# Kernel optimization log

Measured on AMD Instinct MI355X. Metric: run time of the kernel, lower is better.

## Reference

```python
import jax, jax.numpy as jnp
import numpy as np
import math

IN_F, OUT_F = 4096, 4096
ORDER, TENSOR_RANK = 4, 8
LEAF_A = math.ceil(IN_F ** (1.0 / ORDER))   # 8
LEAF_B = math.ceil(OUT_F ** (1.0 / ORDER))  # 8


def setup_inputs() -> dict:
    key = jax.random.key(0)
    k1, k2, k3, k4 = jax.random.split(key, 4)
    x = jax.random.normal(k1, (8, 2048, IN_F), dtype=jnp.float32)
    weight = jax.random.normal(k2, (OUT_F, IN_F), dtype=jnp.float32) * 0.02
    bias = jax.random.normal(k3, (OUT_F,), dtype=jnp.float32) * 0.02
    # reset_parameters: gain for leaky_relu(sqrt(5)) = sqrt(2/(1+5)); std = gain / in_features**(1/order)
    gain = math.sqrt(2.0 / (1.0 + 5.0))
    std = gain / (IN_F ** (1.0 / ORDER))
    weight_leafs = jax.random.uniform(
        k4, (ORDER, TENSOR_RANK, LEAF_A, LEAF_B), dtype=jnp.float32,
        minval=-std, maxval=std)
    return {"x": x, "weight": weight, "bias": bias, "weight_leafs": weight_leafs}


def _reproduce_weight(weight_leafs):
    # Original einsum 'lij,rmn->rimjn' sums the FIRST operand over its leading
    # (rank) axis; chained through both stages + final .sum(0), every leaf is
    # summed over tensor_rank. Exact math = nested Kronecker of the rank-summed
    # leaves, sliced to [:in_features, :out_features].
    s = weight_leafs.sum(axis=1)  # (4, a, b)
    a, b = LEAF_A, LEAF_B
    z1 = jnp.einsum('ij,mn->imjn', s[0], s[1]).reshape(a * a, b * b)
    z2 = jnp.einsum('ij,mn->imjn', s[2], s[3]).reshape(a * a, b * b)
    zzz = jnp.einsum('ij,mn->imjn', z1, z2).reshape(a ** 4, b ** 4)
    return zzz[:IN_F, :OUT_F]  # (in_features, out_features)


def reference(x, weight, bias, weight_leafs):
    tensor_weight = _reproduce_weight(weight_leafs)       # (in, out)
    full_weight = weight + tensor_weight.T                # (out, in)
    # F.linear: x @ W^T + b
    return jnp.einsum('bsi,oi->bso', x, full_weight) + bias
```

## Files before the change

### kernel.cpp

```cpp
#include <hip/hip_runtime.h>
#include <hip/hip_bf16.h>
#include <stdint.h>

typedef __attribute__((ext_vector_type(8))) __bf16 bf16x8;
typedef __attribute__((ext_vector_type(4))) float f32x4;

#define IN_F   4096
#define OUT_F  4096
#define M_ROWS 16384

static __device__ __forceinline__ unsigned short f2bf(float f) {
    unsigned int u = __float_as_uint(f);
    u += 0x7FFFu + ((u >> 16) & 1u);
    return (unsigned short)(u >> 16);
}

__global__ __launch_bounds__(256) void build_w_kernel(
    const float* __restrict__ weight, const float* __restrict__ leafs,
    unsigned short* __restrict__ wb)
{
    __shared__ float s[4][8][8];
    const int t = threadIdx.x;
    {
        const int o = t >> 6, a = (t >> 3) & 7, b = t & 7;
        float acc = 0.f;
        #pragma unroll
        for (int r = 0; r < 8; ++r)
            acc += leafs[o * 512 + r * 64 + a * 8 + b];
        s[o][a][b] = acc;
    }
    __syncthreads();

    const int total = (OUT_F * IN_F) / 8;
    for (int idx = blockIdx.x * 256 + t; idx < total; idx += gridDim.x * 256) {
        const int n  = idx >> 9;
        const int kg = idx & 511;
        const int n0 = n >> 9, n1 = (n >> 6) & 7, n2 = (n >> 3) & 7, n3 = n & 7;
        const int k0 = kg >> 6, k1 = (kg >> 3) & 7, k2 = kg & 7;
        const float p = s[0][k0][n0] * s[1][k1][n1] * s[2][k2][n2];
        const float4* wp = (const float4*)(weight + (size_t)n * IN_F + kg * 8);
        const float4 w0 = wp[0], w1 = wp[1];
        const float wv[8] = {w0.x, w0.y, w0.z, w0.w, w1.x, w1.y, w1.z, w1.w};
        unsigned int pk[4];
        #pragma unroll
        for (int j = 0; j < 4; ++j) {
            unsigned int lo = f2bf(wv[2*j]   + p * s[3][2*j]  [n3]);
            unsigned int hi = f2bf(wv[2*j+1] + p * s[3][2*j+1][n3]);
            pk[j] = lo | (hi << 16);
        }
        *reinterpret_cast<uint4*>(wb + (size_t)n * IN_F + kg * 8) =
            make_uint4(pk[0], pk[1], pk[2], pk[3]);
    }
}

__global__ __launch_bounds__(256) void conv_x_kernel(
    const float* __restrict__ x, unsigned short* __restrict__ xb, long long n8)
{
    for (long long idx = (long long)blockIdx.x * 256 + threadIdx.x; idx < n8;
         idx += (long long)gridDim.x * 256) {
        const float4* xp = (const float4*)(x + idx * 8);
        const float4 a = xp[0], b = xp[1];
        const float v[8] = {a.x, a.y, a.z, a.w, b.x, b.y, b.z, b.w};
        unsigned int pk[4];
        #pragma unroll
        for (int j = 0; j < 4; ++j)
            pk[j] = (unsigned int)f2bf(v[2*j]) | ((unsigned int)f2bf(v[2*j+1]) << 16);
        *reinterpret_cast<uint4*>(xb + idx * 8) = make_uint4(pk[0], pk[1], pk[2], pk[3]);
    }
}

#define BK 64
#define NT 64

#define PANEL_A(b,kk) (ldsb + ((b)*2+(kk))*16384)
#define PANEL_B(b,kk) (ldsb + 65536 + ((b)*2+(kk))*16384)

#define GLL(src, dst) __builtin_amdgcn_global_load_lds( \
    (const __attribute__((address_space(1))) void*)(src), \
    (__attribute__((address_space(3))) void*)(dst), 16, 0, 0)

#define STAGE_A(b, kk, ko) do { \
    GLL(sA1 + (ko) + (kk)*32,          PANEL_A(b,kk) + d1); \
    GLL(sA1 + 524288 + (ko) + (kk)*32, PANEL_A(b,kk) + d1 + 8192); } while(0)
#define STAGE_B(b, kk, ko) do { \
    GLL(sB1 + (ko) + (kk)*32,          PANEL_B(b,kk) + d1); \
    GLL(sB1 + 524288 + (ko) + (kk)*32, PANEL_B(b,kk) + d1 + 8192); } while(0)

#define SB0  __builtin_amdgcn_sched_barrier(0)
#define BAR  __builtin_amdgcn_s_barrier()
#define PRI1 __builtin_amdgcn_s_setprio(1)
#define PRI0 __builtin_amdgcn_s_setprio(0)
#define WLG4 asm volatile("s_waitcnt lgkmcnt(4)" ::: "memory")
#define WLG0 asm volatile("s_waitcnt lgkmcnt(0)" ::: "memory")
#define WVM2 asm volatile("s_waitcnt vmcnt(2)" ::: "memory")
#define WVM0 asm volatile("s_waitcnt vmcnt(0)" ::: "memory")

#define LDA(dst, BUF, KK, MH) do { _Pragma("unroll") \
    for (int i_ = 0; i_ < 4; ++i_) \
        dst[i_] = *(const bf16x8*)(aB + ((BUF)*32768 + (KK)*16384 + ((MH)*4+i_)*1024)); } while(0)
#define LDB(dst, BUF, KK) do { _Pragma("unroll") \
    for (int i_ = 0; i_ < 4; ++i_) \
        dst[i_] = *(const bf16x8*)(bB + ((BUF)*32768 + (KK)*16384 + i_*1024)); } while(0)
#define MM(AS, MH) do { _Pragma("unroll") \
    for (int m_ = 0; m_ < 4; ++m_) { _Pragma("unroll") \
    for (int n_ = 0; n_ < 4; ++n_) \
        acc[(MH)*4+m_][n_] = __builtin_amdgcn_mfma_f32_16x16x32_bf16( \
            AS[m_], bF[n_], acc[(MH)*4+m_][n_], 0, 0, 0); } } while(0)

#define TILE(BUF, KO, PF) do { \
     \
    LDB(bF, BUF, 0); \
    LDA(aQ, BUF, 0, 1); \
    if (PF) STAGE_A((BUF)^1, 0, KO); \
    SB0; WLG4; SB0; \
    PRI1; MM(aP, 0); PRI0; SB0; \
    if (PF) { WVM2; } else { WVM0; } \
    BAR; SB0; \
     \
    LDA(aP, BUF, 1, 0); \
    if (PF) STAGE_B((BUF)^1, 0, KO); \
    SB0; WLG4; SB0; \
    PRI1; MM(aQ, 1); PRI0; SB0; \
    BAR; SB0; \
     \
    LDB(bF, BUF, 1); \
    LDA(aQ, BUF, 1, 1); \
    if (PF) STAGE_A((BUF)^1, 1, KO); \
    SB0; WLG4; SB0; \
    PRI1; MM(aP, 0); PRI0; SB0; \
    if (PF) { WVM2; } else { WVM0; } \
    BAR; SB0; \
     \
    if (PF) { LDA(aP, (BUF)^1, 0, 0); STAGE_B((BUF)^1, 1, KO); SB0; WLG4; } \
    else    { SB0; WLG0; } \
    SB0; \
    PRI1; MM(aQ, 1); PRI0; SB0; \
    BAR; SB0; \
} while (0)

__global__ __launch_bounds__(512, 2) void gemm8_kernel(
    const unsigned short* __restrict__ xb,
    const unsigned short* __restrict__ wb,
    const float* __restrict__ bias,
    float* __restrict__ out)
{
    __shared__ unsigned short lds_us[65536];
    char* const ldsb = (char*)lds_us;

    const int t    = threadIdx.x;
    const int wave = t >> 6;
    const int lane = t & 63;
    const int lr   = lane & 15;
    const int kq   = lane >> 4;
    const int wr   = wave >> 2;
    const int wcn  = wave & 3;
    const int sx   = (lr & 6) << 3;

    const int bid  = blockIdx.x;
    const int swzb = (bid & 7) * 128 + (bid >> 3);
    const int bm   = (swzb >> 4) * 256;
    const int bn   = (swzb & 15) * 256;

    const int c1 = t;
    const int r1 = c1 >> 2;
    const int q1 = ((c1 & 3) * 16) ^ ((r1 & 6) << 3);
    const unsigned short* sA1 = xb + (size_t)(bm + r1) * IN_F + (q1 >> 1);
    const unsigned short* sB1 = wb + (size_t)(bn + r1) * IN_F + (q1 >> 1);
    const int d1 = c1 * 16;

    const char* aB = ldsb + (wr * 128 + lr) * 64 + ((kq * 16) ^ sx);
    const char* bB = ldsb + 65536 + (wcn * 64 + lr) * 64 + ((kq * 16) ^ sx);

    f32x4 acc[8][4] = {};
    bf16x8 aP[4], aQ[4], bF[4];

    STAGE_A(0, 0, 0); STAGE_B(0, 0, 0); STAGE_A(0, 1, 0); STAGE_B(0, 1, 0);
    asm volatile("s_waitcnt vmcnt(4)" ::: "memory");
    BAR; SB0;
    LDA(aP, 0, 0, 0);

    #pragma unroll 1
    for (int tt = 0; tt < NT - 2; tt += 2) {
        const int ko0 = (tt + 1) * BK;
        const int ko1 = (tt + 2) * BK;
        TILE(0, ko0, true);
        TILE(1, ko1, true);
    }
    TILE(0, (NT - 1) * BK, true);
    TILE(1, 0, false);

    #pragma unroll
    for (int n = 0; n < 4; ++n) {
        const int col = bn + wcn * 64 + n * 16 + lr;
        const float bv = bias[col];
        #pragma unroll
        for (int m = 0; m < 8; ++m) {
            const size_t rb = (size_t)(bm + wr * 128 + m * 16 + kq * 4) * OUT_F + col;
            #pragma unroll
            for (int j = 0; j < 4; ++j)
                out[rb + (size_t)j * OUT_F] = acc[m][n][j] + bv;
        }
    }
}

#define FBM 128
#define FBN 128
#define FBK 32

__global__ __launch_bounds__(256) void gemm_fb_kernel(
    const float* __restrict__ xf,
    const unsigned short* __restrict__ wb,
    const float* __restrict__ bias,
    float* __restrict__ out)
{
    __shared__ unsigned short As[FBM * FBK];
    __shared__ unsigned short Bs[FBN * FBK];

    const int t    = threadIdx.x;
    const int wave = t >> 6;
    const int lane = t & 63;
    const int lr   = lane & 15;
    const int kq   = lane >> 4;
    const int wr   = wave >> 1;
    const int wc   = wave & 1;

    const int bm = blockIdx.x * FBM;
    const int bn = blockIdx.y * FBN;
    const int srow = t >> 2;
    const int scol = (t & 3) * 8;

    f32x4 acc[4][4] = {};

    for (int kt = 0; kt < IN_F; kt += FBK) {
        #pragma unroll
        for (int g = 0; g < 2; ++g) {
            const int row = srow + g * 64;
            const float4* xp = (const float4*)(xf + (size_t)(bm + row) * IN_F + kt + scol);
            const float4 a0 = xp[0], a1 = xp[1];
            const float v[8] = {a0.x, a0.y, a0.z, a0.w, a1.x, a1.y, a1.z, a1.w};
            unsigned int pk[4];
            #pragma unroll
            for (int j = 0; j < 4; ++j)
                pk[j] = (unsigned int)f2bf(v[2*j]) | ((unsigned int)f2bf(v[2*j+1]) << 16);
            *reinterpret_cast<uint4*>(&As[row * FBK + scol]) =
                make_uint4(pk[0], pk[1], pk[2], pk[3]);
        }
        {
            const unsigned short* gb0 = wb + (size_t)(bn + srow) * IN_F + kt + scol;
            const unsigned short* gb1 = gb0 + (size_t)64 * IN_F;
            GLL(gb0, Bs + srow * FBK + scol);
            GLL(gb1, Bs + (64 + srow) * FBK + scol);
        }
        __syncthreads();

        bf16x8 af[4], bfr[4];
        #pragma unroll
        for (int m = 0; m < 4; ++m)
            af[m] = *reinterpret_cast<const bf16x8*>(As + (wr * 64 + m * 16 + lr) * FBK + kq * 8);
        #pragma unroll
        for (int n = 0; n < 4; ++n)
            bfr[n] = *reinterpret_cast<const bf16x8*>(Bs + (wc * 64 + n * 16 + lr) * FBK + kq * 8);

        #pragma unroll
        for (int m = 0; m < 4; ++m)
            #pragma unroll
            for (int n = 0; n < 4; ++n)
                acc[m][n] = __builtin_amdgcn_mfma_f32_16x16x32_bf16(af[m], bfr[n], acc[m][n], 0, 0, 0);

        __syncthreads();
    }

    const int crow0 = kq * 4;
    #pragma unroll
    for (int n = 0; n < 4; ++n) {
        const int col = bn + wc * 64 + n * 16 + lr;
        const float bv = bias[col];
        #pragma unroll
        for (int m = 0; m < 4; ++m) {
            const int rowb = bm + wr * 64 + m * 16 + crow0;
            #pragma unroll
            for (int j = 0; j < 4; ++j)
                out[(size_t)(rowb + j) * OUT_F + col] = acc[m][n][j] + bv;
        }
    }
}

extern "C" void kernel_launch(void* const* d_in, const int* in_sizes, int n_in,
                              void* d_out, int out_size, void* d_ws, size_t ws_size,
                              hipStream_t stream) {
    const float* x      = (const float*)d_in[0];
    const float* weight = (const float*)d_in[1];
    const float* bias   = (const float*)d_in[2];
    const float* leafs  = (const float*)d_in[3];
    float* out = (float*)d_out;

    unsigned short* wb = (unsigned short*)d_ws;
    unsigned short* xbuf = (unsigned short*)((char*)d_ws +
                           (size_t)OUT_F * IN_F * sizeof(unsigned short));

    const size_t need_full = (size_t)OUT_F * IN_F * 2 + (size_t)M_ROWS * IN_F * 2;
    const bool full = ws_size >= need_full;

    build_w_kernel<<<dim3(2048), dim3(256), 0, stream>>>(weight, leafs, wb);

    if (full) {
        conv_x_kernel<<<dim3(2048), dim3(256), 0, stream>>>(
            x, xbuf, (long long)M_ROWS * IN_F / 8);
        gemm8_kernel<<<dim3((M_ROWS / 256) * (OUT_F / 256)), dim3(512), 0, stream>>>(
            xbuf, wb, bias, out);
    } else {
        gemm_fb_kernel<<<dim3(M_ROWS / FBM, OUT_F / FBN), dim3(256), 0, stream>>>(
            x, wb, bias, out);
    }
}
```

Measured before the change: 590.2 us.

## Merge weight/x prep kernels and double-buffer B fragments in GEMM

Combines the weight-building and x-conversion kernels into one launch, with blocks split in proportion to the work so both bandwidth-bound conversions run concurrently and one launch and its tail are removed. In the GEMM main loop, B fragments now use two register sets (bP/bQ). Each B load is issued one phase earlier alongside the A loads, and the LDS wait threshold rises to lgkmcnt(8) so more loads stay in flight while MFMAs run. This adds 16 VGPRs per thread, which could pressure the 2-blocks-per-CU occupancy target.

Result: no change. 594.1 us (+0.7%).

```diff
diff --git a/kernel.cpp b/kernel.cpp
--- a/kernel.cpp
+++ b/kernel.cpp
@@ -15,57 +15,62 @@
     return (unsigned short)(u >> 16);
 }
 
-__global__ __launch_bounds__(256) void build_w_kernel(
+#define PREP_WBLK 1366
+#define PREP_NBLK 4096
+
+__global__ __launch_bounds__(256) void prep_kernel(
     const float* __restrict__ weight, const float* __restrict__ leafs,
-    unsigned short* __restrict__ wb)
+    const float* __restrict__ x,
+    unsigned short* __restrict__ wb, unsigned short* __restrict__ xbuf)
 {
-    __shared__ float s[4][8][8];
     const int t = threadIdx.x;
-    {
-        const int o = t >> 6, a = (t >> 3) & 7, b = t & 7;
-        float acc = 0.f;
-        #pragma unroll
-        for (int r = 0; r < 8; ++r)
-            acc += leafs[o * 512 + r * 64 + a * 8 + b];
-        s[o][a][b] = acc;
-    }
-    __syncthreads();
-
-    const int total = (OUT_F * IN_F) / 8;
-    for (int idx = blockIdx.x * 256 + t; idx < total; idx += gridDim.x * 256) {
-        const int n  = idx >> 9;
-        const int kg = idx & 511;
-        const int n0 = n >> 9, n1 = (n >> 6) & 7, n2 = (n >> 3) & 7, n3 = n & 7;
-        const int k0 = kg >> 6, k1 = (kg >> 3) & 7, k2 = kg & 7;
-        const float p = s[0][k0][n0] * s[1][k1][n1] * s[2][k2][n2];
-        const float4* wp = (const float4*)(weight + (size_t)n * IN_F + kg * 8);
-        const float4 w0 = wp[0], w1 = wp[1];
-        const float wv[8] = {w0.x, w0.y, w0.z, w0.w, w1.x, w1.y, w1.z, w1.w};
-        unsigned int pk[4];
-        #pragma unroll
-        for (int j = 0; j < 4; ++j) {
-            unsigned int lo = f2bf(wv[2*j]   + p * s[3][2*j]  [n3]);
-            unsigned int hi = f2bf(wv[2*j+1] + p * s[3][2*j+1][n3]);
-            pk[j] = lo | (hi << 16);
-        }
-        *reinterpret_cast<uint4*>(wb + (size_t)n * IN_F + kg * 8) =
-            make_uint4(pk[0], pk[1], pk[2], pk[3]);
-    }
-}
-
-__global__ __launch_bounds__(256) void conv_x_kernel(
-    const float* __restrict__ x, unsigned short* __restrict__ xb, long long n8)
-{
-    for (long long idx = (long long)blockIdx.x * 256 + threadIdx.x; idx < n8;
-         idx += (long long)gridDim.x * 256) {
-        const float4* xp = (const float4*)(x + idx * 8);
-        const float4 a = xp[0], b = xp[1];
-        const float v[8] = {a.x, a.y, a.z, a.w, b.x, b.y, b.z, b.w};
-        unsigned int pk[4];
-        #pragma unroll
-        for (int j = 0; j < 4; ++j)
-            pk[j] = (unsigned int)f2bf(v[2*j]) | ((unsigned int)f2bf(v[2*j+1]) << 16);
-        *reinterpret_cast<uint4*>(xb + idx * 8) = make_uint4(pk[0], pk[1], pk[2], pk[3]);
+    if (blockIdx.x < PREP_WBLK) {
+        __shared__ float s[4][8][8];
+        {
+            const int o = t >> 6, a = (t >> 3) & 7, b = t & 7;
+            float acc = 0.f;
+            #pragma unroll
+            for (int r = 0; r < 8; ++r)
+                acc += leafs[o * 512 + r * 64 + a * 8 + b];
+            s[o][a][b] = acc;
+        }
+        __syncthreads();
+
+        const int total = (OUT_F * IN_F) / 8;
+        for (int idx = blockIdx.x * 256 + t; idx < total; idx += PREP_WBLK * 256) {
+            const int n  = idx >> 9;
+            const int kg = idx & 511;
+            const int n0 = n >> 9, n1 = (n >> 6) & 7, n2 = (n >> 3) & 7, n3 = n & 7;
+            const int k0 = kg >> 6, k1 = (kg >> 3) & 7, k2 = kg & 7;
+            const float p = s[0][k0][n0] * s[1][k1][n1] * s[2][k2][n2];
+            const float4* wp = (const float4*)(weight + (size_t)n * IN_F + kg * 8);
+            const float4 w0 = wp[0], w1 = wp[1];
+            const float wv[8] = {w0.x, w0.y, w0.z, w0.w, w1.x, w1.y, w1.z, w1.w};
+            unsigned int pk[4];
+            #pragma unroll
+            for (int j = 0; j < 4; ++j) {
+                unsigned int lo = f2bf(wv[2*j]   + p * s[3][2*j]  [n3]);
+                unsigned int hi = f2bf(wv[2*j+1] + p * s[3][2*j+1][n3]);
+                pk[j] = lo | (hi << 16);
+            }
+            *reinterpret_cast<uint4*>(wb + (size_t)n * IN_F + kg * 8) =
+                make_uint4(pk[0], pk[1], pk[2], pk[3]);
+        }
+    } else {
+        const long long n8 = (long long)M_ROWS * IN_F / 8;
+        const int xblocks = PREP_NBLK - PREP_WBLK;
+        for (long long idx = (long long)(blockIdx.x - PREP_WBLK) * 256 + t;
+             idx < n8; idx += (long long)xblocks * 256) {
+            const float4* xp = (const float4*)(x + idx * 8);
+            const float4 a = xp[0], b = xp[1];
+            const float v[8] = {a.x, a.y, a.z, a.w, b.x, b.y, b.z, b.w};
+            unsigned int pk[4];
+            #pragma unroll
+            for (int j = 0; j < 4; ++j)
+                pk[j] = (unsigned int)f2bf(v[2*j]) | ((unsigned int)f2bf(v[2*j+1]) << 16);
+            *reinterpret_cast<uint4*>(xbuf + idx * 8) =
+                make_uint4(pk[0], pk[1], pk[2], pk[3]);
+        }
     }
 }
 
@@ -91,6 +96,7 @@
 #define PRI1 __builtin_amdgcn_s_setprio(1)
 #define PRI0 __builtin_amdgcn_s_setprio(0)
 #define WLG4 asm volatile("s_waitcnt lgkmcnt(4)" ::: "memory")
+#define WLG8 asm volatile("s_waitcnt lgkmcnt(8)" ::: "memory")
 #define WLG0 asm volatile("s_waitcnt lgkmcnt(0)" ::: "memory")
 #define WVM2 asm volatile("s_waitcnt vmcnt(2)" ::: "memory")
 #define WVM0 asm volatile("s_waitcnt vmcnt(0)" ::: "memory")
@@ -101,40 +107,39 @@
 #define LDB(dst, BUF, KK) do { _Pragma("unroll") \
     for (int i_ = 0; i_ < 4; ++i_) \
         dst[i_] = *(const bf16x8*)(bB + ((BUF)*32768 + (KK)*16384 + i_*1024)); } while(0)
-#define MM(AS, MH) do { _Pragma("unroll") \
+#define MMB(AS, BS, MH) do { _Pragma("unroll") \
     for (int m_ = 0; m_ < 4; ++m_) { _Pragma("unroll") \
     for (int n_ = 0; n_ < 4; ++n_) \
         acc[(MH)*4+m_][n_] = __builtin_amdgcn_mfma_f32_16x16x32_bf16( \
-            AS[m_], bF[n_], acc[(MH)*4+m_][n_], 0, 0, 0); } } while(0)
+            AS[m_], BS[n_], acc[(MH)*4+m_][n_], 0, 0, 0); } } while(0)
 
 #define TILE(BUF, KO, PF) do { \
      \
-    LDB(bF, BUF, 0); \
     LDA(aQ, BUF, 0, 1); \
     if (PF) STAGE_A((BUF)^1, 0, KO); \
     SB0; WLG4; SB0; \
-    PRI1; MM(aP, 0); PRI0; SB0; \
+    PRI1; MMB(aP, bP, 0); PRI0; SB0; \
     if (PF) { WVM2; } else { WVM0; } \
     BAR; SB0; \
      \
     LDA(aP, BUF, 1, 0); \
+    LDB(bQ, BUF, 1); \
     if (PF) STAGE_B((BUF)^1, 0, KO); \
-    SB0; WLG4; SB0; \
-    PRI1; MM(aQ, 1); PRI0; SB0; \
+    SB0; WLG8; SB0; \
+    PRI1; MMB(aQ, bP, 1); PRI0; SB0; \
     BAR; SB0; \
      \
-    LDB(bF, BUF, 1); \
     LDA(aQ, BUF, 1, 1); \
     if (PF) STAGE_A((BUF)^1, 1, KO); \
     SB0; WLG4; SB0; \
-    PRI1; MM(aP, 0); PRI0; SB0; \
+    PRI1; MMB(aP, bQ, 0); PRI0; SB0; \
     if (PF) { WVM2; } else { WVM0; } \
     BAR; SB0; \
      \
-    if (PF) { LDA(aP, (BUF)^1, 0, 0); STAGE_B((BUF)^1, 1, KO); SB0; WLG4; } \
+    if (PF) { LDA(aP, (BUF)^1, 0, 0); LDB(bP, (BUF)^1, 0); STAGE_B((BUF)^1, 1, KO); SB0; WLG8; } \
     else    { SB0; WLG0; } \
     SB0; \
-    PRI1; MM(aQ, 1); PRI0; SB0; \
+    PRI1; MMB(aQ, bQ, 1); PRI0; SB0; \
     BAR; SB0; \
 } while (0)
 
@@ -172,12 +177,13 @@
     const char* bB = ldsb + 65536 + (wcn * 64 + lr) * 64 + ((kq * 16) ^ sx);
 
     f32x4 acc[8][4] = {};
-    bf16x8 aP[4], aQ[4], bF[4];
+    bf16x8 aP[4], aQ[4], bP[4], bQ[4];
 
     STAGE_A(0, 0, 0); STAGE_B(0, 0, 0); STAGE_A(0, 1, 0); STAGE_B(0, 1, 0);
     asm volatile("s_waitcnt vmcnt(4)" ::: "memory");
     BAR; SB0;
     LDA(aP, 0, 0, 0);
+    LDB(bP, 0, 0);
 
     #pragma unroll 1
     for (int tt = 0; tt < NT - 2; tt += 2) {
@@ -301,14 +307,14 @@
     const size_t need_full = (size_t)OUT_F * IN_F * 2 + (size_t)M_ROWS * IN_F * 2;
     const bool full = ws_size >= need_full;
 
-    build_w_kernel<<<dim3(2048), dim3(256), 0, stream>>>(weight, leafs, wb);
-
     if (full) {
-        conv_x_kernel<<<dim3(2048), dim3(256), 0, stream>>>(
-            x, xbuf, (long long)M_ROWS * IN_F / 8);
+        prep_kernel<<<dim3(PREP_NBLK), dim3(256), 0, stream>>>(
+            weight, leafs, x, wb, xbuf);
         gemm8_kernel<<<dim3((M_ROWS / 256) * (OUT_F / 256)), dim3(512), 0, stream>>>(
             xbuf, wb, bias, out);
     } else {
+        prep_kernel<<<dim3(PREP_WBLK), dim3(256), 0, stream>>>(
+            weight, leafs, x, wb, xbuf);
         gemm_fb_kernel<<<dim3(M_ROWS / FBM, OUT_F / FBN), dim3(256), 0, stream>>>(
             x, wb, bias, out);
     }
```
